# Kernel tuning notes

Hardware: AMD Instinct MI355X
Metric: run time of the kernel (lower is better)

## Reference

```python
import jax, jax.numpy as jnp
import numpy as np

N_NODES = 100000
N_EDGES = 1600000
IN_F = 128
HID_F = 128
N_CLS = 40


def _linear_params(key, out_f, in_f):
    k1, k2 = jax.random.split(key)
    s = 1.0 / np.sqrt(in_f)
    w = jax.random.uniform(k1, (out_f, in_f), jnp.float32, -s, s)
    b = jax.random.uniform(k2, (out_f,), jnp.float32, -s, s)
    return w, b


def setup_inputs() -> dict:
    key = jax.random.key(0)
    ks = jax.random.split(key, 9)
    in_feat = jax.random.normal(ks[0], (N_NODES, IN_F), jnp.float32)
    src = jax.random.randint(ks[1], (N_EDGES,), 0, N_NODES, jnp.int32)
    dst = jax.random.randint(ks[2], (N_EDGES,), 0, N_NODES, jnp.int32)
    pool_w1, pool_b1 = _linear_params(ks[3], IN_F, IN_F)
    self_w1, self_b1 = _linear_params(ks[4], HID_F, IN_F)
    neigh_w1, neigh_b1 = _linear_params(ks[5], HID_F, IN_F)
    pool_w2, pool_b2 = _linear_params(ks[6], HID_F, HID_F)
    self_w2, self_b2 = _linear_params(ks[7], N_CLS, HID_F)
    neigh_w2, neigh_b2 = _linear_params(ks[8], N_CLS, HID_F)
    return dict(in_feat=in_feat, src=src, dst=dst,
                pool_w1=pool_w1, pool_b1=pool_b1, self_w1=self_w1, self_b1=self_b1,
                neigh_w1=neigh_w1, neigh_b1=neigh_b1,
                pool_w2=pool_w2, pool_b2=pool_b2, self_w2=self_w2, self_b2=self_b2,
                neigh_w2=neigh_w2, neigh_b2=neigh_b2)


def sage_conv_pool(h, src, dst, pool_w, pool_b, self_w, self_b, neigh_w, neigh_b):
    # fc_pool + relu on nodes first (N < E), then gather per edge
    m = jax.nn.relu(h @ pool_w.T + pool_b)            # [N, d]
    msgs = m[src]                                     # [E, d] gather
    agg = jax.ops.segment_max(msgs, dst, num_segments=N_NODES)  # [N, d]
    agg = jnp.where(jnp.isfinite(agg), agg, 0.0)      # zero for isolated nodes
    return h @ self_w.T + self_b + agg @ neigh_w.T + neigh_b


def reference(in_feat, src, dst,
              pool_w1, pool_b1, self_w1, self_b1, neigh_w1, neigh_b1,
              pool_w2, pool_b2, self_w2, self_b2, neigh_w2, neigh_b2):
    h = sage_conv_pool(in_feat, src, dst, pool_w1, pool_b1, self_w1, self_b1, neigh_w1, neigh_b1)
    h = jax.nn.relu(h)  # dropout is identity in eval mode
    h = sage_conv_pool(h, src, dst, pool_w2, pool_b2, self_w2, self_b2, neigh_w2, neigh_b2)
    return h
```

## Files before the change

kernel.cpp:

```cpp
#include <hip/hip_runtime.h>


#define N_FEAT 128
#define NWG_A 256
#define BSHIFT 10
#define NBMAX 128

typedef __attribute__((ext_vector_type(8))) short bf16x8;
typedef __attribute__((ext_vector_type(8))) unsigned short u16x8;
typedef __attribute__((ext_vector_type(4))) float f32x4;

static __device__ __forceinline__ unsigned short f2bf(float f) {
    unsigned u = __float_as_uint(f);
    unsigned r = (u + 0x7fffu + ((u >> 16) & 1u)) >> 16;
    return (unsigned short)r;
}

static __device__ __forceinline__ bf16x8 loadA_f32(const float* __restrict__ A, size_t idx) {
    float4 a = *(const float4*)&A[idx];
    float4 b = *(const float4*)&A[idx + 4];
    bf16x8 r;
    r[0] = (short)f2bf(a.x); r[1] = (short)f2bf(a.y);
    r[2] = (short)f2bf(a.z); r[3] = (short)f2bf(a.w);
    r[4] = (short)f2bf(b.x); r[5] = (short)f2bf(b.y);
    r[6] = (short)f2bf(b.z); r[7] = (short)f2bf(b.w);
    return r;
}

__global__ __launch_bounds__(256) void prep_bin_kernel(
    const float* __restrict__ pw1, const float* __restrict__ sw1,
    const float* __restrict__ nw1, const float* __restrict__ pw2,
    const float* __restrict__ sw2, const float* __restrict__ nw2,
    const float* __restrict__ sb1, const float* __restrict__ nb1,
    const float* __restrict__ sb2, const float* __restrict__ nb2,
    unsigned short* __restrict__ wb_p1, unsigned short* __restrict__ wb_s1,
    unsigned short* __restrict__ wb_n1, unsigned short* __restrict__ wb_p2,
    unsigned short* __restrict__ wb_s2, unsigned short* __restrict__ wb_n2,
    float* __restrict__ b_sn1, float* __restrict__ b_sn2,
    const int* __restrict__ dst, int* __restrict__ wgcnt, int E, int NB)
{
    __shared__ int cnt[NBMAX];
    if (blockIdx.x < NWG_A) {
        const int wg = blockIdx.x, tid = threadIdx.x;
        if (tid < NB) cnt[tid] = 0;
        __syncthreads();
        const int slab = (E + NWG_A - 1) / NWG_A;
        const int e0 = wg * slab;
        const int e1 = min(e0 + slab, E);
        for (int e = e0 + tid; e < e1; e += 256)
            atomicAdd(&cnt[dst[e] >> BSHIFT], 1);
        __syncthreads();
        if (tid < NB) wgcnt[tid * NWG_A + wg] = cnt[tid];
    } else {
        int t = (blockIdx.x - NWG_A) * 256 + threadIdx.x;
        if (t < 16384) {
            wb_p1[t] = f2bf(pw1[t]);
            wb_s1[t] = f2bf(sw1[t]);
            wb_n1[t] = f2bf(nw1[t]);
            wb_p2[t] = f2bf(pw2[t]);
        }
        if (t < 6144) {
            int row = t >> 7;
            wb_s2[t] = (row < 40) ? f2bf(sw2[t]) : 0;
            wb_n2[t] = (row < 40) ? f2bf(nw2[t]) : 0;
        }
        if (t < 128) b_sn1[t] = sb1[t] + nb1[t];
        if (t < 64)  b_sn2[t] = (t < 40) ? (sb2[t] + nb2[t]) : 0.f;
    }
}

__global__ __launch_bounds__(256) void bin_scan_kernel(const int* __restrict__ wgcnt,
                                                       int* __restrict__ binoff, int NB)
{
    __shared__ int sh[256];
    const int t = threadIdx.x;
    const int base = t * NB;
    int s = 0;
    for (int k = 0; k < NB; k++) s += wgcnt[base + k];
    sh[t] = s;
    __syncthreads();
    for (int off = 1; off < 256; off <<= 1) {
        int x = (t >= off) ? sh[t - off] : 0;
        __syncthreads();
        sh[t] += x;
        __syncthreads();
    }
    int run = sh[t] - s;
    for (int k = 0; k < NB; k++) {
        int v = wgcnt[base + k];
        binoff[base + k] = run;
        run += v;
    }
    if (t == 255) binoff[NB * NWG_A] = run;
}

__global__ __launch_bounds__(256) void bin_scatter_kernel(const int* __restrict__ src,
                                                          const int* __restrict__ dst,
                                                          const int* __restrict__ binoff,
                                                          unsigned* __restrict__ binned,
                                                          int E, int NB)
{
    __shared__ int cur[NBMAX];
    const int wg = blockIdx.x, tid = threadIdx.x;
    if (tid < NB) cur[tid] = binoff[tid * NWG_A + wg];
    __syncthreads();
    const int slab = (E + NWG_A - 1) / NWG_A;
    const int e0 = wg * slab;
    const int e1 = min(e0 + slab, E);
    for (int e = e0 + tid; e < e1; e += 256) {
        int d = dst[e];
        int b = d >> BSHIFT;
        unsigned rec = ((unsigned)(d & ((1 << BSHIFT) - 1)) << 17) | (unsigned)src[e];
        int p = atomicAdd(&cur[b], 1);
        binned[p] = rec;
    }
}

__global__ __launch_bounds__(256) void csr_build_kernel(const unsigned* __restrict__ binned,
                                                        const int* __restrict__ binoff,
                                                        int* __restrict__ csr,
                                                        int* __restrict__ offsets,
                                                        int* __restrict__ counts, int M)
{
    __shared__ int cnt[1 << BSHIFT];
    __shared__ int scn[1 << BSHIFT];
    __shared__ int sh[256];
    const int b = blockIdx.x, t = threadIdx.x;
    const int rs = binoff[b * NWG_A];
    const int re = binoff[(b + 1) * NWG_A];

    for (int j = t; j < (1 << BSHIFT); j += 256) cnt[j] = 0;
    __syncthreads();
    for (int i = rs + t; i < re; i += 256)
        atomicAdd(&cnt[binned[i] >> 17], 1);
    __syncthreads();

    const int base4 = t * 4;
    int v[4];
#pragma unroll
    for (int k = 0; k < 4; k++) v[k] = cnt[base4 + k];
    int s = v[0] + v[1] + v[2] + v[3];
    sh[t] = s;
    __syncthreads();
    for (int off = 1; off < 256; off <<= 1) {
        int x = (t >= off) ? sh[t - off] : 0;
        __syncthreads();
        sh[t] += x;
        __syncthreads();
    }
    int run = sh[t] - s;
#pragma unroll
    for (int k = 0; k < 4; k++) {
        scn[base4 + k] = run;
        run += v[k];
    }

    const int node0 = b << BSHIFT;
#pragma unroll
    for (int k = 0; k < 4; k++) {
        int j = base4 + k;
        int node = node0 + j;
        if (node < M) {
            counts[node] = v[k];
            offsets[node] = rs + scn[j];
        }
    }
    __syncthreads();

    for (int i = rs + t; i < re; i += 256) {
        unsigned r = binned[i];
        int p = atomicAdd(&scn[r >> 17], 1);
        csr[rs + p] = (int)(r & 0x1FFFFu);
    }
}

__global__ __launch_bounds__(256) void gather_max_kernel(
    const u16x8* __restrict__ m16, const int* __restrict__ csr,
    const int* __restrict__ offsets, const int* __restrict__ counts,
    u16x8* __restrict__ agg16, int Nn)
{
    int wid = (blockIdx.x * 256 + threadIdx.x) >> 6;
    int lane = threadIdx.x & 63;
    if (wid >= Nn) return;
    const int g = lane >> 4, c = lane & 15;
    int start = offsets[wid];
    int deg = counts[wid];
    u16x8 acc = (u16x8){0, 0, 0, 0, 0, 0, 0, 0};
    for (int j0 = 0; j0 < deg; j0 += 64) {
        int nb = deg - j0;
        if (nb > 64) nb = 64;
        int sl = csr[start + j0 + (lane < nb ? lane : nb - 1)];
        for (int j = 0; j < nb; j += 4) {
            int jj = j + g;
            if (jj >= nb) jj = nb - 1;
            int s = __shfl(sl, jj);
            u16x8 v = m16[(size_t)s * 16 + c];
            acc = __builtin_elementwise_max(acc, v);
        }
    }
#pragma unroll
    for (int d = 16; d <= 32; d <<= 1) {
        int4 a = *(int4*)&acc;
        int4 t;
        t.x = __shfl_xor(a.x, d);
        t.y = __shfl_xor(a.y, d);
        t.z = __shfl_xor(a.z, d);
        t.w = __shfl_xor(a.w, d);
        acc = __builtin_elementwise_max(acc, *(u16x8*)&t);
    }
    if (g == 0) agg16[(size_t)wid * 16 + c] = acc;
}

template<int NT, bool RELU, int NPAIRS, bool A0F32, bool F32OUT>
__global__ __launch_bounds__(256, 4) void mfma_gemm_kernel(
    const void* __restrict__ A0v, const unsigned short* __restrict__ B0,
    const unsigned short* __restrict__ A1, const unsigned short* __restrict__ B1,
    const float* __restrict__ bias, void* __restrict__ Cout, int M, int Nout)
{
    constexpr int NR = NT * 16;
    __shared__ unsigned short Bs[NR * 136];
    __shared__ float BsF[NR];

    const int tid = threadIdx.x;
    const int w = tid >> 6, lane = tid & 63;
    const int q = lane >> 4, r16 = lane & 15;
    const int m0 = blockIdx.x * 128;

    if (tid < NR) BsF[tid] = (tid < Nout) ? bias[tid] : 0.f;

    int rowA[2];
#pragma unroll
    for (int rt = 0; rt < 2; rt++) {
        int r = m0 + w * 32 + rt * 16 + r16;
        rowA[rt] = r < M ? r : (M - 1);
    }

    f32x4 acc[2][NT];
#pragma unroll
    for (int i = 0; i < 2; i++)
#pragma unroll
        for (int j = 0; j < NT; j++) acc[i][j] = (f32x4){0.f, 0.f, 0.f, 0.f};

    for (int p = 0; p < NPAIRS; p++) {
        const unsigned short* __restrict__ B = p ? B1 : B0;
        if (p) __syncthreads();
        for (int j = tid; j < NR * 16; j += 256) {
            int row = j >> 4, cc = j & 15;
            uint4 v = *(const uint4*)&B[(size_t)row * 128 + cc * 8];
            *(uint4*)&Bs[row * 136 + cc * 8] = v;
        }
        __syncthreads();

#pragma unroll
        for (int k0 = 0; k0 < 128; k0 += 32) {
            bf16x8 af[2];
#pragma unroll
            for (int rt = 0; rt < 2; rt++) {
                if (p == 0 && A0F32)
                    af[rt] = loadA_f32((const float*)A0v, (size_t)rowA[rt] * 128 + k0 + q * 8);
                else {
                    const unsigned short* Ab = p ? A1 : (const unsigned short*)A0v;
                    af[rt] = *(const bf16x8*)&Ab[(size_t)rowA[rt] * 128 + k0 + q * 8];
                }
            }
#pragma unroll
            for (int ct = 0; ct < NT; ct++) {
                bf16x8 bfr = *(const bf16x8*)&Bs[(ct * 16 + r16) * 136 + k0 + q * 8];
#pragma unroll
                for (int rt = 0; rt < 2; rt++)
                    acc[rt][ct] = __builtin_amdgcn_mfma_f32_16x16x32_bf16(
                        af[rt], bfr, acc[rt][ct], 0, 0, 0);
            }
        }
    }

#pragma unroll
    for (int rt = 0; rt < 2; rt++) {
#pragma unroll
        for (int ct = 0; ct < NT; ct++) {
            int col = ct * 16 + r16;
#pragma unroll
            for (int r = 0; r < 4; r++) {
                int grow = m0 + w * 32 + rt * 16 + q * 4 + r;
                float v = acc[rt][ct][r] + BsF[col];
                if (RELU) v = fmaxf(v, 0.f);
                if (grow < M && col < Nout) {
                    if (F32OUT)
                        ((float*)Cout)[(size_t)grow * Nout + col] = v;
                    else
                        ((unsigned short*)Cout)[(size_t)grow * Nout + col] = f2bf(v);
                }
            }
        }
    }
}

__global__ __launch_bounds__(256, 2) void sn_pool_kernel(
    const float* __restrict__ A0f, const unsigned short* __restrict__ B0,
    const unsigned short* __restrict__ A1, const unsigned short* __restrict__ B1,
    const float* __restrict__ bias_sn, const unsigned short* __restrict__ Bp,
    const float* __restrict__ bias_p, unsigned short* __restrict__ h1out,
    unsigned short* __restrict__ m2out, int M)
{
    __shared__ unsigned short Bs[128 * 136];
    __shared__ unsigned short H[128 * 136];
    __shared__ float BsF[128];

    const int tid = threadIdx.x;
    const int w = tid >> 6, lane = tid & 63;
    const int q = lane >> 4, r16 = lane & 15;
    const int m0 = blockIdx.x * 128;

    if (tid < 128) BsF[tid] = bias_sn[tid];

    int rowA[2];
#pragma unroll
    for (int rt = 0; rt < 2; rt++) {
        int r = m0 + w * 32 + rt * 16 + r16;
        rowA[rt] = r < M ? r : (M - 1);
    }

    f32x4 acc[2][8];
#pragma unroll
    for (int i = 0; i < 2; i++)
#pragma unroll
        for (int j = 0; j < 8; j++) acc[i][j] = (f32x4){0.f, 0.f, 0.f, 0.f};

    for (int j = tid; j < 2048; j += 256) {
        int row = j >> 4, cc = j & 15;
        *(uint4*)&Bs[row * 136 + cc * 8] = *(const uint4*)&B0[(size_t)row * 128 + cc * 8];
    }
    __syncthreads();
#pragma unroll
    for (int k0 = 0; k0 < 128; k0 += 32) {
        bf16x8 af[2];
#pragma unroll
        for (int rt = 0; rt < 2; rt++)
            af[rt] = loadA_f32(A0f, (size_t)rowA[rt] * 128 + k0 + q * 8);
#pragma unroll
        for (int ct = 0; ct < 8; ct++) {
            bf16x8 bfr = *(const bf16x8*)&Bs[(ct * 16 + r16) * 136 + k0 + q * 8];
#pragma unroll
            for (int rt = 0; rt < 2; rt++)
                acc[rt][ct] = __builtin_amdgcn_mfma_f32_16x16x32_bf16(
                    af[rt], bfr, acc[rt][ct], 0, 0, 0);
        }
    }
    __syncthreads();

    for (int j = tid; j < 2048; j += 256) {
        int row = j >> 4, cc = j & 15;
        *(uint4*)&Bs[row * 136 + cc * 8] = *(const uint4*)&B1[(size_t)row * 128 + cc * 8];
    }
    __syncthreads();
#pragma unroll
    for (int k0 = 0; k0 < 128; k0 += 32) {
        bf16x8 af[2];
#pragma unroll
        for (int rt = 0; rt < 2; rt++)
            af[rt] = *(const bf16x8*)&A1[(size_t)rowA[rt] * 128 + k0 + q * 8];
#pragma unroll
        for (int ct = 0; ct < 8; ct++) {
            bf16x8 bfr = *(const bf16x8*)&Bs[(ct * 16 + r16) * 136 + k0 + q * 8];
#pragma unroll
            for (int rt = 0; rt < 2; rt++)
                acc[rt][ct] = __builtin_amdgcn_mfma_f32_16x16x32_bf16(
                    af[rt], bfr, acc[rt][ct], 0, 0, 0);
        }
    }

#pragma unroll
    for (int rt = 0; rt < 2; rt++) {
#pragma unroll
        for (int ct = 0; ct < 8; ct++) {
            int col = ct * 16 + r16;
#pragma unroll
            for (int r = 0; r < 4; r++) {
                int lr = w * 32 + rt * 16 + q * 4 + r;
                int grow = m0 + lr;
                float v = fmaxf(acc[rt][ct][r] + BsF[col], 0.f);
                unsigned short hb = f2bf(v);
                H[lr * 136 + col] = hb;
                if (grow < M) h1out[(size_t)grow * 128 + col] = hb;
            }
        }
    }
    __syncthreads();

    for (int j = tid; j < 2048; j += 256) {
        int row = j >> 4, cc = j & 15;
        *(uint4*)&Bs[row * 136 + cc * 8] = *(const uint4*)&Bp[(size_t)row * 128 + cc * 8];
    }
    if (tid < 128) BsF[tid] = bias_p[tid];
    __syncthreads();

#pragma unroll
    for (int i = 0; i < 2; i++)
#pragma unroll
        for (int j = 0; j < 8; j++) acc[i][j] = (f32x4){0.f, 0.f, 0.f, 0.f};

#pragma unroll
    for (int k0 = 0; k0 < 128; k0 += 32) {
        bf16x8 af[2];
#pragma unroll
        for (int rt = 0; rt < 2; rt++)
            af[rt] = *(const bf16x8*)&H[(w * 32 + rt * 16 + r16) * 136 + k0 + q * 8];
#pragma unroll
        for (int ct = 0; ct < 8; ct++) {
            bf16x8 bfr = *(const bf16x8*)&Bs[(ct * 16 + r16) * 136 + k0 + q * 8];
#pragma unroll
            for (int rt = 0; rt < 2; rt++)
                acc[rt][ct] = __builtin_amdgcn_mfma_f32_16x16x32_bf16(
                    af[rt], bfr, acc[rt][ct], 0, 0, 0);
        }
    }

#pragma unroll
    for (int rt = 0; rt < 2; rt++) {
#pragma unroll
        for (int ct = 0; ct < 8; ct++) {
            int col = ct * 16 + r16;
#pragma unroll
            for (int r = 0; r < 4; r++) {
                int grow = m0 + w * 32 + rt * 16 + q * 4 + r;
                if (grow < M) {
                    float v = fmaxf(acc[rt][ct][r] + BsF[col], 0.f);
                    m2out[(size_t)grow * 128 + col] = f2bf(v);
                }
            }
        }
    }
}

extern "C" void kernel_launch(void* const* d_in, const int* in_sizes, int n_in,
                              void* d_out, int out_size, void* d_ws, size_t ws_size,
                              hipStream_t stream)
{
    const float* in_feat = (const float*)d_in[0];
    const int*   src     = (const int*)d_in[1];
    const int*   dst     = (const int*)d_in[2];
    const float* pw1 = (const float*)d_in[3];  const float* pb1 = (const float*)d_in[4];
    const float* sw1 = (const float*)d_in[5];  const float* sb1 = (const float*)d_in[6];
    const float* nw1 = (const float*)d_in[7];  const float* nb1 = (const float*)d_in[8];
    const float* pw2 = (const float*)d_in[9];  const float* pb2 = (const float*)d_in[10];
    const float* sw2 = (const float*)d_in[11]; const float* sb2 = (const float*)d_in[12];
    const float* nw2 = (const float*)d_in[13]; const float* nb2 = (const float*)d_in[14];
    float* out = (float*)d_out;

    const int M = in_sizes[0] / N_FEAT;
    const int E = in_sizes[1];
    const int NB = (M + (1 << BSHIFT) - 1) >> BSHIFT;

    char* base = (char*)d_ws;
    size_t off = 0;
    auto alloc = [&](size_t bytes) { char* p = base + off; off = (off + bytes + 255) & ~(size_t)255; return p; };
    unsigned short* wb_p1 = (unsigned short*)alloc(16384 * 2);
    unsigned short* wb_s1 = (unsigned short*)alloc(16384 * 2);
    unsigned short* wb_n1 = (unsigned short*)alloc(16384 * 2);
    unsigned short* wb_p2 = (unsigned short*)alloc(16384 * 2);
    unsigned short* wb_s2 = (unsigned short*)alloc(6144 * 2);
    unsigned short* wb_n2 = (unsigned short*)alloc(6144 * 2);
    float* b_sn1 = (float*)alloc(128 * 4);
    float* b_sn2 = (float*)alloc(64 * 4);
    unsigned short* mb   = (unsigned short*)alloc((size_t)M * 128 * 2);
    unsigned short* agg  = (unsigned short*)alloc((size_t)M * 128 * 2);
    unsigned short* h1   = (unsigned short*)alloc((size_t)M * 128 * 2);
    int* counts  = (int*)alloc((size_t)M * 4);
    int* offsets = (int*)alloc((size_t)M * 4);
    int* wgcnt   = (int*)alloc((size_t)NB * NWG_A * 4);
    int* binoff  = (int*)alloc(((size_t)NB * NWG_A + 1) * 4);
    unsigned* binned = (unsigned*)alloc((size_t)E * 4);
    int* csr     = (int*)alloc((size_t)E * 4);

    const int gemm_grid = (M + 127) / 128;
    const int gather_grid = (M * 64 + 255) / 256;

    prep_bin_kernel<<<NWG_A + 64, 256, 0, stream>>>(
        pw1, sw1, nw1, pw2, sw2, nw2, sb1, nb1, sb2, nb2,
        wb_p1, wb_s1, wb_n1, wb_p2, wb_s2, wb_n2, b_sn1, b_sn2,
        dst, wgcnt, E, NB);
    bin_scan_kernel<<<1, 256, 0, stream>>>(wgcnt, binoff, NB);
    bin_scatter_kernel<<<NWG_A, 256, 0, stream>>>(src, dst, binoff, binned, E, NB);
    csr_build_kernel<<<NB, 256, 0, stream>>>(binned, binoff, csr, offsets, counts, M);

    mfma_gemm_kernel<8, true, 1, true, false><<<gemm_grid, 256, 0, stream>>>(
        in_feat, wb_p1, nullptr, nullptr, pb1, mb, M, 128);
    gather_max_kernel<<<gather_grid, 256, 0, stream>>>(
        (const u16x8*)mb, csr, offsets, counts, (u16x8*)agg, M);
    sn_pool_kernel<<<gemm_grid, 256, 0, stream>>>(
        in_feat, wb_s1, agg, wb_n1, b_sn1, wb_p2, pb2, h1, mb, M);

    gather_max_kernel<<<gather_grid, 256, 0, stream>>>(
        (const u16x8*)mb, csr, offsets, counts, (u16x8*)agg, M);
    mfma_gemm_kernel<3, false, 2, false, true><<<gemm_grid, 256, 0, stream>>>(
        h1, wb_s2, agg, wb_n2, b_sn2, out, M, 40);
}
```

Before: 393.8 us.

## Fuse edge scatter with first pool GEMM and widen scan/CSR kernels

Merges the edge bin-scatter pass and the first pool-projection GEMM into one launch, with separate block ranges for each, so the scatter and the GEMM can run concurrently and one launch disappears. The single-block bin scan and the per-bin CSR build now use 1024 threads, so the CSR build needs one scan element per thread instead of four. Non-temporal stores are used for the binned records and the aggregated features. The fused kernel reserves GEMM-sized shared memory even for scatter blocks, which may reduce occupancy for that part.

```diff
diff --git a/kernel.cpp b/kernel.cpp
--- a/kernel.cpp
+++ b/kernel.cpp
@@ -69,107 +69,160 @@
     }
 }
 
-__global__ __launch_bounds__(256) void bin_scan_kernel(const int* __restrict__ wgcnt,
-                                                       int* __restrict__ binoff, int NB)
-{
-    __shared__ int sh[256];
+__global__ __launch_bounds__(1024) void bin_scan_kernel(const int* __restrict__ wgcnt,
+                                                        int* __restrict__ binoff, int NB)
+{
+    __shared__ int sh[1024];
     const int t = threadIdx.x;
-    const int base = t * NB;
+    const int total = NB * NWG_A;
+    const int chunk = (total + 1023) / 1024;
+    const int b0 = t * chunk;
+    const int b1 = min(b0 + chunk, total);
     int s = 0;
-    for (int k = 0; k < NB; k++) s += wgcnt[base + k];
+    for (int k = b0; k < b1; k++) s += wgcnt[k];
     sh[t] = s;
     __syncthreads();
-    for (int off = 1; off < 256; off <<= 1) {
+    for (int off = 1; off < 1024; off <<= 1) {
         int x = (t >= off) ? sh[t - off] : 0;
         __syncthreads();
         sh[t] += x;
         __syncthreads();
     }
     int run = sh[t] - s;
-    for (int k = 0; k < NB; k++) {
-        int v = wgcnt[base + k];
-        binoff[base + k] = run;
+    for (int k = b0; k < b1; k++) {
+        int v = wgcnt[k];
+        binoff[k] = run;
         run += v;
     }
-    if (t == 255) binoff[NB * NWG_A] = run;
-}
-
-__global__ __launch_bounds__(256) void bin_scatter_kernel(const int* __restrict__ src,
-                                                          const int* __restrict__ dst,
-                                                          const int* __restrict__ binoff,
-                                                          unsigned* __restrict__ binned,
-                                                          int E, int NB)
+    if (t == 1023) binoff[total] = sh[1023];
+}
+
+__global__ __launch_bounds__(256, 4) void scatter_pool_kernel(
+    const int* __restrict__ src, const int* __restrict__ dst,
+    const int* __restrict__ binoff, unsigned* __restrict__ binned, int E, int NB,
+    const float* __restrict__ A0f, const unsigned short* __restrict__ B0,
+    const float* __restrict__ bias, unsigned short* __restrict__ Cout, int M)
 {
     __shared__ int cur[NBMAX];
-    const int wg = blockIdx.x, tid = threadIdx.x;
-    if (tid < NB) cur[tid] = binoff[tid * NWG_A + wg];
-    __syncthreads();
-    const int slab = (E + NWG_A - 1) / NWG_A;
-    const int e0 = wg * slab;
-    const int e1 = min(e0 + slab, E);
-    for (int e = e0 + tid; e < e1; e += 256) {
-        int d = dst[e];
-        int b = d >> BSHIFT;
-        unsigned rec = ((unsigned)(d & ((1 << BSHIFT) - 1)) << 17) | (unsigned)src[e];
-        int p = atomicAdd(&cur[b], 1);
-        binned[p] = rec;
-    }
-}
-
-__global__ __launch_bounds__(256) void csr_build_kernel(const unsigned* __restrict__ binned,
-                                                        const int* __restrict__ binoff,
-                                                        int* __restrict__ csr,
-                                                        int* __restrict__ offsets,
-                                                        int* __restrict__ counts, int M)
+    __shared__ unsigned short Bs[128 * 136];
+    __shared__ float BsF[128];
+
+    if (blockIdx.x < NWG_A) {
+        const int wg = blockIdx.x, tid = threadIdx.x;
+        if (tid < NB) cur[tid] = binoff[tid * NWG_A + wg];
+        __syncthreads();
+        const int slab = (E + NWG_A - 1) / NWG_A;
+        const int e0 = wg * slab;
+        const int e1 = min(e0 + slab, E);
+        for (int e = e0 + tid; e < e1; e += 256) {
+            int d = dst[e];
+            int b = d >> BSHIFT;
+            unsigned rec = ((unsigned)(d & ((1 << BSHIFT) - 1)) << 17) | (unsigned)src[e];
+            int p = atomicAdd(&cur[b], 1);
+            __builtin_nontemporal_store(rec, &binned[p]);
+        }
+        return;
+    }
+
+    const int tid = threadIdx.x;
+    const int w = tid >> 6, lane = tid & 63;
+    const int q = lane >> 4, r16 = lane & 15;
+    const int m0 = (blockIdx.x - NWG_A) * 128;
+
+    if (tid < 128) BsF[tid] = bias[tid];
+
+    int rowA[2];
+#pragma unroll
+    for (int rt = 0; rt < 2; rt++) {
+        int r = m0 + w * 32 + rt * 16 + r16;
+        rowA[rt] = r < M ? r : (M - 1);
+    }
+
+    f32x4 acc[2][8];
+#pragma unroll
+    for (int i = 0; i < 2; i++)
+#pragma unroll
+        for (int j = 0; j < 8; j++) acc[i][j] = (f32x4){0.f, 0.f, 0.f, 0.f};
+
+    for (int j = tid; j < 2048; j += 256) {
+        int row = j >> 4, cc = j & 15;
+        *(uint4*)&Bs[row * 136 + cc * 8] = *(const uint4*)&B0[(size_t)row * 128 + cc * 8];
+    }
+    __syncthreads();
+
+#pragma unroll
+    for (int k0 = 0; k0 < 128; k0 += 32) {
+        bf16x8 af[2];
+#pragma unroll
+        for (int rt = 0; rt < 2; rt++)
+            af[rt] = loadA_f32(A0f, (size_t)rowA[rt] * 128 + k0 + q * 8);
+#pragma unroll
+        for (int ct = 0; ct < 8; ct++) {
+            bf16x8 bfr = *(const bf16x8*)&Bs[(ct * 16 + r16) * 136 + k0 + q * 8];
+#pragma unroll
+            for (int rt = 0; rt < 2; rt++)
+                acc[rt][ct] = __builtin_amdgcn_mfma_f32_16x16x32_bf16(
+                    af[rt], bfr, acc[rt][ct], 0, 0, 0);
+        }
+    }
+
+#pragma unroll
+    for (int rt = 0; rt < 2; rt++) {
+#pragma unroll
+        for (int ct = 0; ct < 8; ct++) {
+            int col = ct * 16 + r16;
+#pragma unroll
+            for (int r = 0; r < 4; r++) {
+                int grow = m0 + w * 32 + rt * 16 + q * 4 + r;
+                if (grow < M) {
+                    float v = fmaxf(acc[rt][ct][r] + BsF[col], 0.f);
+                    Cout[(size_t)grow * 128 + col] = f2bf(v);
+                }
+            }
+        }
+    }
+}
+
+__global__ __launch_bounds__(1024) void csr_build_kernel(const unsigned* __restrict__ binned,
+                                                         const int* __restrict__ binoff,
+                                                         int* __restrict__ csr,
+                                                         int* __restrict__ offsets,
+                                                         int* __restrict__ counts, int M)
 {
     __shared__ int cnt[1 << BSHIFT];
-    __shared__ int scn[1 << BSHIFT];
-    __shared__ int sh[256];
+    __shared__ int pref[1 << BSHIFT];
     const int b = blockIdx.x, t = threadIdx.x;
     const int rs = binoff[b * NWG_A];
     const int re = binoff[(b + 1) * NWG_A];
 
-    for (int j = t; j < (1 << BSHIFT); j += 256) cnt[j] = 0;
-    __syncthreads();
-    for (int i = rs + t; i < re; i += 256)
+    cnt[t] = 0;
+    __syncthreads();
+    for (int i = rs + t; i < re; i += 1024)
         atomicAdd(&cnt[binned[i] >> 17], 1);
     __syncthreads();
 
-    const int base4 = t * 4;
-    int v[4];
-#pragma unroll
-    for (int k = 0; k < 4; k++) v[k] = cnt[base4 + k];
-    int s = v[0] + v[1] + v[2] + v[3];
-    sh[t] = s;
-    __syncthreads();
-    for (int off = 1; off < 256; off <<= 1) {
-        int x = (t >= off) ? sh[t - off] : 0;
-        __syncthreads();
-        sh[t] += x;
-        __syncthreads();
-    }
-    int run = sh[t] - s;
-#pragma unroll
-    for (int k = 0; k < 4; k++) {
-        scn[base4 + k] = run;
-        run += v[k];
-    }
-
-    const int node0 = b << BSHIFT;
-#pragma unroll
-    for (int k = 0; k < 4; k++) {
-        int j = base4 + k;
-        int node = node0 + j;
-        if (node < M) {
-            counts[node] = v[k];
-            offsets[node] = rs + scn[j];
-        }
-    }
-    __syncthreads();
-
-    for (int i = rs + t; i < re; i += 256) {
+    int v = cnt[t];
+    pref[t] = v;
+    __syncthreads();
+    for (int off = 1; off < 1024; off <<= 1) {
+        int x = (t >= off) ? pref[t - off] : 0;
+        __syncthreads();
+        pref[t] += x;
+        __syncthreads();
+    }
+    int excl = pref[t] - v;
+
+    int node = (b << BSHIFT) + t;
+    if (node < M) {
+        counts[node] = v;
+        offsets[node] = rs + excl;
+    }
+    cnt[t] = excl;
+    __syncthreads();
+
+    for (int i = rs + t; i < re; i += 1024) {
         unsigned r = binned[i];
-        int p = atomicAdd(&scn[r >> 17], 1);
+        int p = atomicAdd(&cnt[r >> 17], 1);
         csr[rs + p] = (int)(r & 0x1FFFFu);
     }
 }
@@ -208,12 +261,12 @@
         t.w = __shfl_xor(a.w, d);
         acc = __builtin_elementwise_max(acc, *(u16x8*)&t);
     }
-    if (g == 0) agg16[(size_t)wid * 16 + c] = acc;
-}
-
-template<int NT, bool RELU, int NPAIRS, bool A0F32, bool F32OUT>
+    if (g == 0) __builtin_nontemporal_store(acc, &agg16[(size_t)wid * 16 + c]);
+}
+
+template<int NT, bool RELU, int NPAIRS, bool F32OUT>
 __global__ __launch_bounds__(256, 4) void mfma_gemm_kernel(
-    const void* __restrict__ A0v, const unsigned short* __restrict__ B0,
+    const unsigned short* __restrict__ A0, const unsigned short* __restrict__ B0,
     const unsigned short* __restrict__ A1, const unsigned short* __restrict__ B1,
     const float* __restrict__ bias, void* __restrict__ Cout, int M, int Nout)
 {
@@ -243,6 +296,7 @@
 
     for (int p = 0; p < NPAIRS; p++) {
         const unsigned short* __restrict__ B = p ? B1 : B0;
+        const unsigned short* __restrict__ A = p ? A1 : A0;
         if (p) __syncthreads();
         for (int j = tid; j < NR * 16; j += 256) {
             int row = j >> 4, cc = j & 15;
@@ -255,14 +309,8 @@
         for (int k0 = 0; k0 < 128; k0 += 32) {
             bf16x8 af[2];
 #pragma unroll
-            for (int rt = 0; rt < 2; rt++) {
-                if (p == 0 && A0F32)
-                    af[rt] = loadA_f32((const float*)A0v, (size_t)rowA[rt] * 128 + k0 + q * 8);
-                else {
-                    const unsigned short* Ab = p ? A1 : (const unsigned short*)A0v;
-                    af[rt] = *(const bf16x8*)&Ab[(size_t)rowA[rt] * 128 + k0 + q * 8];
-                }
-            }
+            for (int rt = 0; rt < 2; rt++)
+                af[rt] = *(const bf16x8*)&A[(size_t)rowA[rt] * 128 + k0 + q * 8];
 #pragma unroll
             for (int ct = 0; ct < NT; ct++) {
                 bf16x8 bfr = *(const bf16x8*)&Bs[(ct * 16 + r16) * 136 + k0 + q * 8];
@@ -479,12 +527,12 @@
         pw1, sw1, nw1, pw2, sw2, nw2, sb1, nb1, sb2, nb2,
         wb_p1, wb_s1, wb_n1, wb_p2, wb_s2, wb_n2, b_sn1, b_sn2,
         dst, wgcnt, E, NB);
-    bin_scan_kernel<<<1, 256, 0, stream>>>(wgcnt, binoff, NB);
-    bin_scatter_kernel<<<NWG_A, 256, 0, stream>>>(src, dst, binoff, binned, E, NB);
-    csr_build_kernel<<<NB, 256, 0, stream>>>(binned, binoff, csr, offsets, counts, M);
-
-    mfma_gemm_kernel<8, true, 1, true, false><<<gemm_grid, 256, 0, stream>>>(
-        in_feat, wb_p1, nullptr, nullptr, pb1, mb, M, 128);
+    bin_scan_kernel<<<1, 1024, 0, stream>>>(wgcnt, binoff, NB);
+    scatter_pool_kernel<<<NWG_A + gemm_grid, 256, 0, stream>>>(
+        src, dst, binoff, binned, E, NB,
+        in_feat, wb_p1, pb1, mb, M);
+    csr_build_kernel<<<NB, 1024, 0, stream>>>(binned, binoff, csr, offsets, counts, M);
+
     gather_max_kernel<<<gather_grid, 256, 0, stream>>>(
         (const u16x8*)mb, csr, offsets, counts, (u16x8*)agg, M);
     sn_pool_kernel<<<gemm_grid, 256, 0, stream>>>(
@@ -492,6 +540,6 @@
 
     gather_max_kernel<<<gather_grid, 256, 0, stream>>>(
         (const u16x8*)mb, csr, offsets, counts, (u16x8*)agg, M);
-    mfma_gemm_kernel<3, false, 2, false, true><<<gemm_grid, 256, 0, stream>>>(
+    mfma_gemm_kernel<3, false, 2, true><<<gemm_grid, 256, 0, stream>>>(
         h1, wb_s2, agg, wb_n2, b_sn2, out, M, 40);
 }
```

Measured after the change: 391.6 us. Within noise of the previous version (-0.6%).
